# Kernel tuning notes

Measured on AMD Instinct MI355X. Metric: run time of the kernel, lower is better.

The kernel has to match this reference:

```python
import jax, jax.numpy as jnp
import numpy as np
from jax.ops import segment_sum, segment_max

N_NODES, N_EDGES, D_IN, D_H, D_E, HEADS, LAYERS, D_OUT, N_GRAPHS = 50000, 150000, 48, 64, 16, 10, 3, 128, 4096


def setup_inputs() -> dict:
    key = jax.random.key(0)
    ks = jax.random.split(key, 24)
    x = jax.random.normal(ks[0], (N_NODES, D_IN), jnp.float32)
    edge_attr = jax.random.uniform(ks[1], (N_EDGES, D_E), jnp.float32)
    edge_index = jax.random.randint(ks[2], (2, N_EDGES), 0, N_NODES, dtype=jnp.int32)
    batch_ids = jnp.sort(jax.random.randint(ks[3], (N_NODES,), 0, N_GRAPHS, dtype=jnp.int32))
    s = 0.05
    W_emb = jax.random.normal(ks[4], (D_IN, D_H), jnp.float32) * s
    b_emb = jnp.zeros((D_H,), jnp.float32)
    Ws = jax.random.normal(ks[5], (LAYERS, D_H, HEADS * D_H), jnp.float32) * s
    att_src = jax.random.normal(ks[6], (LAYERS, HEADS, D_H), jnp.float32) * s
    att_dst = jax.random.normal(ks[7], (LAYERS, HEADS, D_H), jnp.float32) * s
    att_edge = jax.random.normal(ks[8], (LAYERS, HEADS, D_H), jnp.float32) * s
    W_edge = jax.random.normal(ks[9], (LAYERS, D_E, HEADS * D_H), jnp.float32) * s
    bias = jnp.zeros((LAYERS, D_H), jnp.float32)
    bn_gamma = jnp.ones((LAYERS, D_H), jnp.float32)
    bn_beta = jnp.zeros((LAYERS, D_H), jnp.float32)
    bn_mean = jax.random.normal(ks[10], (LAYERS, D_H), jnp.float32) * 0.1
    bn_var = jax.random.uniform(ks[11], (LAYERS, D_H), jnp.float32) + 0.5
    W_out = jax.random.normal(ks[12], (D_H, D_OUT), jnp.float32) * s
    b_out = jnp.zeros((D_OUT,), jnp.float32)
    return dict(x=x, edge_attr=edge_attr, W_emb=W_emb, b_emb=b_emb, Ws=Ws,
                att_src=att_src, att_dst=att_dst, att_edge=att_edge, W_edge=W_edge,
                bias=bias, bn_gamma=bn_gamma, bn_beta=bn_beta, bn_mean=bn_mean,
                bn_var=bn_var, W_out=W_out, b_out=b_out,
                edge_index=edge_index, batch_ids=batch_ids)


def reference(x, edge_attr, W_emb, b_emb, Ws, att_src, att_dst, att_edge, W_edge,
              bias, bn_gamma, bn_beta, bn_mean, bn_var, W_out, b_out,
              edge_index, batch_ids):
    N = x.shape[0]
    H, F = att_src.shape[1], att_src.shape[2]
    src, dst = edge_index[0], edge_index[1]
    # PyG add_self_loops(fill_value='mean'): self-loop edge_attr = scatter-mean of incoming edge_attr
    cnt = segment_sum(jnp.ones(src.shape, jnp.float32), dst, num_segments=N)
    loop_attr = segment_sum(edge_attr, dst, num_segments=N) / jnp.maximum(cnt, 1.0)[:, None]
    ar = jnp.arange(N, dtype=src.dtype)
    src2 = jnp.concatenate([src, ar])
    dst2 = jnp.concatenate([dst, ar])
    ea2 = jnp.concatenate([edge_attr, loop_attr], axis=0)  # [E+N, De]

    h = x @ W_emb + b_emb  # [N, D_H]
    for i in range(Ws.shape[0]):
        xp = (h @ Ws[i]).reshape(N, H, F)                       # [N,H,F]
        a_s = jnp.einsum('nhf,hf->nh', xp, att_src[i])
        a_d = jnp.einsum('nhf,hf->nh', xp, att_dst[i])
        ep = (ea2 @ W_edge[i]).reshape(-1, H, F)                # [E2,H,F]
        a_e = jnp.einsum('ehf,hf->eh', ep, att_edge[i])
        alpha = jax.nn.leaky_relu(a_s[src2] + a_d[dst2] + a_e, 0.2)  # [E2,H]
        m = segment_max(alpha, dst2, num_segments=N)            # segment softmax over dst
        e = jnp.exp(alpha - m[dst2])
        z = segment_sum(e, dst2, num_segments=N)
        att = e / z[dst2]                                       # [E2,H]
        agg = segment_sum(xp[src2] * att[:, :, None], dst2, num_segments=N)  # [N,H,F]
        xc = agg.mean(axis=1) + bias[i]                         # concat=False -> head mean
        xc = (xc - bn_mean[i]) * bn_gamma[i] / jnp.sqrt(bn_var[i] + 1e-5) + bn_beta[i]
        xc = jax.nn.gelu(xc, approximate=False)
        h = h + xc                                              # residual_connection == 'res'
    out = h @ W_out + b_out                                     # [N, D_OUT]
    gsum = segment_sum(out, batch_ids, num_segments=N_GRAPHS)
    gcnt = segment_sum(jnp.ones((N,), jnp.float32), batch_ids, num_segments=N_GRAPHS)
    return gsum / jnp.maximum(gcnt, 1.0)[:, None]               # global_mean_pool [G, D_OUT]
```

## Files before the change

### kernel.cpp

```cpp
#include <hip/hip_runtime.h>
#include <hip/hip_fp16.h>
#include <math.h>

constexpr int NN   = 50000;
constexpr int NE   = 150000;
constexpr int DIN  = 48;
constexpr int DH   = 64;
constexpr int DE   = 16;
constexpr int NHD  = 10;
constexpr int NL   = 3;
constexpr int DOUTC= 128;
constexpr int NG   = 4096;
constexpr int E2   = NE + NN;
constexpr int SCAN_B  = 256;
constexpr int SCAN_NB = (NN + SCAN_B - 1) / SCAN_B;

typedef __bf16 v8bf __attribute__((ext_vector_type(8)));
typedef short  v8s  __attribute__((ext_vector_type(8)));
typedef float  v4f  __attribute__((ext_vector_type(4)));

__device__ inline unsigned short f2bf(float f) {
    unsigned u = __builtin_bit_cast(unsigned, f);
    unsigned r = (u + 0x7FFFu + ((u >> 16) & 1u)) >> 16;
    return (unsigned short)r;
}

__device__ inline v4f MF(v8s a, v8s b, v4f c) {
    return __builtin_amdgcn_mfma_f32_16x16x32_bf16(
        __builtin_bit_cast(v8bf, a), __builtin_bit_cast(v8bf, b), c, 0, 0, 0);
}
__device__ inline v4f MFB(v8bf a, v8s b, v4f c) {
    return __builtin_amdgcn_mfma_f32_16x16x32_bf16(
        a, __builtin_bit_cast(v8bf, b), c, 0, 0, 0);
}

#define RLI(v, l) __builtin_amdgcn_readlane((v), (l))
#define RLH2(v, l) __builtin_bit_cast(__half2, __builtin_amdgcn_readlane(__builtin_bit_cast(int, (v)), (l)))

__global__ void k_zero(int* __restrict__ cnt) {
    int i = blockIdx.x * blockDim.x + threadIdx.x;
    if (i < NN) cnt[i] = 0;
}

__global__ void k_cnt(const int* __restrict__ dst, int* __restrict__ cnt) {
    int e = blockIdx.x * blockDim.x + threadIdx.x;
    if (e < NE) atomicAdd(&cnt[dst[e]], 1);
}

__global__ void k_scan_a(const int* __restrict__ cnt, int* __restrict__ bsum) {
    __shared__ int s[SCAN_B];
    int i = blockIdx.x * SCAN_B + threadIdx.x;
    s[threadIdx.x] = (i < NN) ? (cnt[i] + 1) : 0;
    __syncthreads();
    for (int off = SCAN_B / 2; off > 0; off >>= 1) {
        if (threadIdx.x < off) s[threadIdx.x] += s[threadIdx.x + off];
        __syncthreads();
    }
    if (threadIdx.x == 0) bsum[blockIdx.x] = s[0];
}

__global__ void k_scan_c(const int* __restrict__ cnt, const int* __restrict__ bsum,
                         int* __restrict__ rp, int* __restrict__ cursor) {
    __shared__ int s[SCAN_B];
    __shared__ int boff_s;
    const int t = threadIdx.x;
    int partial = (t < SCAN_NB && t < blockIdx.x) ? bsum[t] : 0;
    s[t] = partial;
    __syncthreads();
    for (int off = SCAN_B / 2; off > 0; off >>= 1) {
        if (t < off) s[t] += s[t + off];
        __syncthreads();
    }
    if (t == 0) boff_s = s[0];
    __syncthreads();
    const int boff = boff_s;
    __syncthreads();
    int i = blockIdx.x * SCAN_B + t;
    if (i < NN) cursor[i] = 0;
    int v = (i < NN) ? (cnt[i] + 1) : 0;
    s[t] = v;
    __syncthreads();
    for (int off = 1; off < SCAN_B; off <<= 1) {
        int tv = (t >= off) ? s[t - off] : 0;
        __syncthreads();
        s[t] += tv;
        __syncthreads();
    }
    if (i < NN) {
        int excl = boff + s[t] - v;
        rp[i] = excl;
        if (i == NN - 1) rp[NN] = excl + v;
    }
}

__global__ void k_csr_fill(const int* __restrict__ src, const int* __restrict__ dst,
                           const int* __restrict__ rp, int* __restrict__ cursor,
                           int* __restrict__ eidx, int* __restrict__ scsr) {
    int e = blockIdx.x * blockDim.x + threadIdx.x;
    if (e >= E2) return;
    int d  = (e < NE) ? dst[e] : (e - NE);
    int sn = (e < NE) ? src[e] : d;
    int pos = atomicAdd(&cursor[d], 1);
    int s = rp[d] + pos;
    eidx[s] = e; scsr[s] = sn;
}

__global__ void k_misc(const int* __restrict__ rp, const int* __restrict__ scsr,
                       const int* __restrict__ eidx, const int* __restrict__ cnt,
                       const float* __restrict__ ea, const int* __restrict__ batch,
                       int* __restrict__ snl12, int* __restrict__ grp,
                       float* __restrict__ loop) {
    int tid = blockIdx.x * blockDim.x + threadIdx.x;
    if (tid < NN * 16) {
        int n = tid >> 4, j = tid & 15;
        int r0 = rp[n], deg = rp[n + 1] - r0;
        int v;
        if (j < 12)      v = (j < deg) ? scsr[r0 + j] : 0;
        else if (j == 12) v = deg;
        else if (j == 13) v = r0;
        else             v = 0;
        snl12[tid] = v;
    } else if (tid < NN * 17) {
        int n = tid - NN * 16;
        int b = batch[n];
        int pb = (n == 0) ? -1 : batch[n - 1];
        for (int g = pb + 1; g <= b; ++g) grp[g] = n;
        if (n == NN - 1) for (int g = b + 1; g <= NG; ++g) grp[g] = NN;
    } else if (tid < NN * 33) {
        int t = tid - NN * 17;
        int n = t >> 4, d = t & 15;
        int r0 = rp[n], r1 = rp[n + 1];
        float s = 0.f;
        for (int q = r0; q < r1; ++q) {
            int eid = eidx[q];
            if (eid < NE) s += ea[(size_t)eid * DE + d];
        }
        int c = cnt[n];
        loop[t] = s * ((c > 1) ? (1.0f / (float)c) : 1.0f);
    }
}

constexpr int N_BTP = NL * 40960;
constexpr int N_WCB = NL * 2048;
constexpr int N_EMB = DH * 64;
constexpr int N_WET = NL * DE * NHD;
__global__ void k_prep(const float* __restrict__ Ws, const float* __restrict__ asrc,
                       const float* __restrict__ adst, const float* __restrict__ We_in,
                       const float* __restrict__ aedge, const float* __restrict__ Wemb,
                       unsigned short* __restrict__ BtP, unsigned short* __restrict__ WcB,
                       unsigned short* __restrict__ BH, unsigned short* __restrict__ BL,
                       float* __restrict__ WeT) {
    int tid = blockIdx.x * blockDim.x + threadIdx.x;
    if (tid < N_BTP) {
        int e  = tid & 7;
        int ln = (tid >> 3) & 63;
        int t  = (tid >> 9) % 20;
        int ct = (tid / 10240) & 3;
        int l  = tid / 40960;
        int f = ct * 16 + (ln & 15);
        int kidx = t * 32 + (ln >> 4) * 8 + e;
        int k = kidx / 10, q = kidx - 10 * (kidx / 10);
        float v = Ws[((size_t)l * DH + k) * 640 + q * 64 + f] * 0.1f;
        BtP[tid] = f2bf(v);
    } else if (tid < N_BTP + N_WCB) {
        int r0 = tid - N_BTP;
        int l = r0 / 2048, r = r0 % 2048;
        int tile = r / 1024, rr = r % 1024;
        int ln = rr / 16, idx = rr % 16;
        int t2 = idx / 8, e = idx % 8;
        int k = t2 * 32 + (ln >> 4) * 8 + e;
        int jc = ln & 15;
        int j = tile * 16 + jc;
        float v = 0.f;
        if (j < 20) {
            int hh = j % NHD;
            const float* a = ((j < NHD) ? asrc : adst) + (size_t)l * NHD * DH + hh * DH;
            const float* w = Ws + ((size_t)l * DH + k) * 640 + hh * DH;
            float s = 0.f;
#pragma unroll
            for (int f = 0; f < DH; ++f) s += w[f] * a[f];
            v = s;
        }
        WcB[r0] = f2bf(v);
    } else if (tid < N_BTP + N_WCB + N_EMB) {
        int r0 = tid - N_BTP - N_WCB;
        int c = r0 >> 6, k = r0 & 63;
        float v = (k < DIN) ? Wemb[(size_t)k * DH + c] : 0.f;
        __bf16 hi = (__bf16)v;
        BH[r0] = __builtin_bit_cast(unsigned short, hi);
        BL[r0] = __builtin_bit_cast(unsigned short, (__bf16)(v - (float)hi));
    } else if (tid < N_BTP + N_WCB + N_EMB + N_WET) {
        int t3 = tid - N_BTP - N_WCB - N_EMB;
        int l = t3 / 160, rr = t3 % 160;
        int hh = rr / 16, d = rr % 16;
        const float* a = aedge + (size_t)l * NHD * DH + hh * DH;
        const float* w = We_in + ((size_t)l * DE + d) * 640 + hh * DH;
        float s = 0.f;
#pragma unroll
        for (int f = 0; f < DH; ++f) s += w[f] * a[f];
        WeT[l * 160 + hh * 16 + d] = s;
    }
}

__global__ void k_ae3(const float* __restrict__ ea, const float* __restrict__ loop,
                      const float* __restrict__ WeT, const int* __restrict__ eidx,
                      __half* __restrict__ aeAll) {
    int tid = blockIdx.x * blockDim.x + threadIdx.x;
    if (tid >= NL * E2 * NHD) return;
    int l = tid / (E2 * NHD);
    int r = tid - l * (E2 * NHD);
    int s = r / NHD, h = r - (r / NHD) * NHD;
    int eid = eidx[s];
    const float* ar = (eid < NE) ? (ea + (size_t)eid * DE) : (loop + (size_t)(eid - NE) * DE);
    const float* wt = WeT + l * 160 + h * 16;
    float4 a0 = *(const float4*)(ar + 0);
    float4 a1 = *(const float4*)(ar + 4);
    float4 a2 = *(const float4*)(ar + 8);
    float4 a3 = *(const float4*)(ar + 12);
    float4 w0 = *(const float4*)(wt + 0);
    float4 w1 = *(const float4*)(wt + 4);
    float4 w2 = *(const float4*)(wt + 8);
    float4 w3 = *(const float4*)(wt + 12);
    float v = a0.x*w0.x + a0.y*w0.y + a0.z*w0.z + a0.w*w0.w
            + a1.x*w1.x + a1.y*w1.y + a1.z*w1.z + a1.w*w1.w
            + a2.x*w2.x + a2.y*w2.y + a2.z*w2.z + a2.w*w2.w
            + a3.x*w3.x + a3.y*w3.y + a3.z*w3.z + a3.w*w3.w;
    aeAll[tid] = (__half)v;
}

__global__ __launch_bounds__(256) void k_emb(const float* __restrict__ x,
        const unsigned short* __restrict__ BH, const unsigned short* __restrict__ BL,
        const float* __restrict__ bemb, const unsigned short* __restrict__ WcB,
        float* __restrict__ h, __half* __restrict__ hh, float* __restrict__ S) {
    __shared__ __align__(16) unsigned short hlb[4][16 * 72];
    const int tid = threadIdx.x;
    const int w = tid >> 6, lane = tid & 63;
    const int la = lane & 15, lb = lane >> 4;
    const int rowbase = blockIdx.x * 64 + w * 16;
    const int nA = rowbase + la;

    v8bf ah[2], al[2];
#pragma unroll
    for (int ks = 0; ks < 2; ++ks) {
        const int k0 = ks * 32 + lb * 8;
        float xv[8];
        if (nA < NN && k0 < DIN) {
            const float* xp = x + (size_t)nA * DIN + k0;
            float4 v0 = *(const float4*)xp;
            float4 v1 = *(const float4*)(xp + 4);
            xv[0]=v0.x; xv[1]=v0.y; xv[2]=v0.z; xv[3]=v0.w;
            xv[4]=v1.x; xv[5]=v1.y; xv[6]=v1.z; xv[7]=v1.w;
        } else {
#pragma unroll
            for (int e = 0; e < 8; ++e) xv[e] = 0.f;
        }
#pragma unroll
        for (int e = 0; e < 8; ++e) {
            __bf16 hi = (__bf16)xv[e];
            ah[ks][e] = hi;
            al[ks][e] = (__bf16)(xv[e] - (float)hi);
        }
    }
    v4f acc[4];
#pragma unroll
    for (int ct = 0; ct < 4; ++ct) acc[ct] = (v4f){0.f, 0.f, 0.f, 0.f};
#pragma unroll
    for (int ct = 0; ct < 4; ++ct) {
#pragma unroll
        for (int ks = 0; ks < 2; ++ks) {
            const int boff = (ct * 16 + la) * 64 + ks * 32 + lb * 8;
            v8s bh = *(const v8s*)&BH[boff];
            v8s bl = *(const v8s*)&BL[boff];
            acc[ct] = MFB(ah[ks], bh, acc[ct]);
            acc[ct] = MFB(al[ks], bh, acc[ct]);
            acc[ct] = MFB(ah[ks], bl, acc[ct]);
        }
    }
#pragma unroll
    for (int ct = 0; ct < 4; ++ct) {
        const int c = ct * 16 + la;
        const float bi = bemb[c];
#pragma unroll
        for (int r = 0; r < 4; ++r) {
            const int row = lb * 4 + r;
            const int n = rowbase + row;
            float v = acc[ct][r] + bi;
            if (n < NN) {
                h[(size_t)n * DH + c] = v;
                hh[(size_t)n * DH + c] = (__half)v;
            }
            hlb[w][row * 72 + c] = f2bf(v);
        }
    }
    __syncthreads();
    v4f s0 = {0.f,0.f,0.f,0.f}, s1 = {0.f,0.f,0.f,0.f};
#pragma unroll
    for (int t = 0; t < 2; ++t) {
        v8s av = *(const v8s*)&hlb[w][la * 72 + t * 32 + lb * 8];
        v8s b0 = *(const v8s*)&WcB[(size_t)(lane) * 16 + t * 8];
        v8s b1 = *(const v8s*)&WcB[(size_t)(64 + lane) * 16 + t * 8];
        s0 = MF(av, b0, s0);
        s1 = MF(av, b1, s1);
    }
#pragma unroll
    for (int r = 0; r < 4; ++r) {
        const int n = rowbase + lb * 4 + r;
        if (n < NN) {
            S[(size_t)n * 20 + la] = s0[r];
            if (la < 4) S[(size_t)n * 20 + 16 + la] = s1[r];
        }
    }
}

__global__ __launch_bounds__(256) void k_layer(
        const float* __restrict__ Sin, const __half* __restrict__ ae,
        __half* __restrict__ wraw,
        const int* __restrict__ snl12, const int* __restrict__ scsr,
        const float* __restrict__ hin, const __half* __restrict__ hinh,
        const unsigned short* __restrict__ BtP, const unsigned short* __restrict__ WcB,
        int do_s, float* __restrict__ Sout,
        const float* __restrict__ bias, const float* __restrict__ gam,
        const float* __restrict__ bet, const float* __restrict__ mean,
        const float* __restrict__ var, float* __restrict__ hout,
        __half* __restrict__ houth) {
    __shared__ __align__(16) unsigned short Gl[16 * 648];
    __shared__ __align__(8)  __half wL[16 * 120];

    const int tid = threadIdx.x;
    const int w = tid >> 6, lane = tid & 63;
    const int blk = blockIdx.x;
    const int nb4 = blk * 16 + w * 4;
    const unsigned* wrawu = (const unsigned*)wraw;

    const int meta = snl12[nb4 * 16 + lane];

    __half hv[4][6];
#pragma unroll
    for (int i = 0; i < 4; ++i) {
#pragma unroll
        for (int j = 0; j < 6; ++j) {
            int sv = RLI(meta, i * 16 + j);
            hv[i][j] = hinh[(size_t)sv * DH + lane];
        }
    }

    if (tid < 160) {
        const int li = tid / 10, h = tid - (tid / 10) * 10;
        const int n = blk * 16 + li;
        const int* mrow = &snl12[n * 16];
        const int deg = mrow[12];
        const int r0  = mrow[13];
        const float sd = Sin[(size_t)n * 20 + 10 + h];
        float aL[12];
        float m = -1e30f;
#pragma unroll
        for (int s = 0; s < 12; ++s) {
            float a = -1e30f;
            if (s < deg) {
                int sn = mrow[s];
                a = Sin[(size_t)sn * 20 + h] + sd + (float)ae[(size_t)(r0 + s) * NHD + h];
                a = (a > 0.f) ? a : 0.2f * a;
                m = fmaxf(m, a);
            }
            aL[s] = a;
        }
        for (int s = 12; s < deg; ++s) {
            int sn = scsr[r0 + s];
            float a = Sin[(size_t)sn * 20 + h] + sd + (float)ae[(size_t)(r0 + s) * NHD + h];
            a = (a > 0.f) ? a : 0.2f * a;
            wraw[(size_t)(r0 + s) * NHD + h] = (__half)a;
            m = fmaxf(m, a);
        }
        float z = 0.f;
#pragma unroll
        for (int s = 0; s < 12; ++s) {
            float e = (s < deg) ? __expf(aL[s] - m) : 0.f;
            aL[s] = e;
            z += e;
        }
        for (int s = 12; s < deg; ++s) {
            float e = __expf((float)wraw[(size_t)(r0 + s) * NHD + h] - m);
            wraw[(size_t)(r0 + s) * NHD + h] = (__half)e;
            z += e;
        }
        float zi = 1.f / z;
#pragma unroll
        for (int s = 0; s < 12; ++s)
            wL[li * 120 + s * 10 + h] = (__half)(aL[s] * zi);
        for (int s = 12; s < deg; ++s)
            wraw[(size_t)(r0 + s) * NHD + h] =
                (__half)((float)wraw[(size_t)(r0 + s) * NHD + h] * zi);
    }
    __syncthreads();

    const unsigned* wLu = (const unsigned*)wL;
    int wfu[4];
#pragma unroll
    for (int i = 0; i < 4; ++i)
        wfu[i] = (int)wLu[(w * 4 + i) * 60 + (lane & 31)];
#pragma unroll
    for (int i = 0; i < 4; ++i) {
        const int li = w * 4 + i;
        const int deg = RLI(meta, i * 16 + 12);
        const int r0  = RLI(meta, i * 16 + 13);
        __half2 g[5];
#pragma unroll
        for (int p = 0; p < 5; ++p) g[p] = __half2{(__half)0.f, (__half)0.f};
#pragma unroll
        for (int j = 0; j < 6; ++j) {
            __half2 hvd = __half2half2(hv[i][j]);
#pragma unroll
            for (int p = 0; p < 5; ++p)
                g[p] = __hfma2(RLH2(wfu[i], j * 5 + p), hvd, g[p]);
        }
        if (deg > 6) {
            {
                int w2 = (lane < 30) ? (int)wLu[li * 60 + 30 + lane] : 0;
                __half hv2[6];
#pragma unroll
                for (int j = 0; j < 6; ++j) {
                    int sv = RLI(meta, i * 16 + 6 + j);
                    hv2[j] = hinh[(size_t)sv * DH + lane];
                }
#pragma unroll
                for (int j = 0; j < 6; ++j) {
                    __half2 hvd = __half2half2(hv2[j]);
#pragma unroll
                    for (int p = 0; p < 5; ++p)
                        g[p] = __hfma2(RLH2(w2, j * 5 + p), hvd, g[p]);
                }
            }
            for (int c0 = 12; c0 < deg; c0 += 6) {
                const int rem = deg - c0;
                int w2 = (lane < 30 && (lane / 5) < rem)
                         ? (int)wrawu[(size_t)(r0 + c0) * 5 + lane] : 0;
                int s2 = (lane < 6 && c0 + lane < deg) ? scsr[r0 + c0 + lane] : 0;
                __half hv2[6];
#pragma unroll
                for (int j = 0; j < 6; ++j) {
                    int sv = RLI(s2, j);
                    hv2[j] = hinh[(size_t)sv * DH + lane];
                }
#pragma unroll
                for (int j = 0; j < 6; ++j) {
                    __half2 hvd = __half2half2(hv2[j]);
#pragma unroll
                    for (int p = 0; p < 5; ++p)
                        g[p] = __hfma2(RLH2(w2, j * 5 + p), hvd, g[p]);
                }
            }
        }
        const int base = li * 648 + lane * 10;
#pragma unroll
        for (int p = 0; p < 5; ++p) {
            float f0 = __low2float(g[p]), f1 = __high2float(g[p]);
            unsigned u = (unsigned)f2bf(f0) | ((unsigned)f2bf(f1) << 16);
            *(unsigned*)&Gl[base + 2 * p] = u;
        }
    }
    __syncthreads();

    const int la = lane & 15, lb = lane >> 4;
    v4f acc = {0.f, 0.f, 0.f, 0.f};
    const unsigned short* bp = BtP + (size_t)w * 20 * 512;
#pragma unroll 5
    for (int t = 0; t < 20; ++t) {
        v8s av = *(const v8s*)&Gl[la * 648 + t * 32 + lb * 8];
        v8s bv = *(const v8s*)&bp[t * 512 + lane * 8];
        acc = MF(av, bv, acc);
    }
    __syncthreads();

    unsigned short* hlb = Gl;
    const int f = w * 16 + la;
    const float bi = bias[f], gm = gam[f], bt_ = bet[f], mu = mean[f];
    const float iv = rsqrtf(var[f] + 1e-5f);
#pragma unroll
    for (int r = 0; r < 4; ++r) {
        const int local = lb * 4 + r;
        const int n = blk * 16 + local;
        float hvold = hin[(size_t)n * DH + f];
        float v = acc[r] + bi;
        v = (v - mu) * gm * iv + bt_;
        v = 0.5f * v * (1.0f + erff(v * 0.70710678118654752f));
        float hnew = hvold + v;
        hout[(size_t)n * DH + f] = hnew;
        houth[(size_t)n * DH + f] = (__half)hnew;
        hlb[local * 72 + f] = f2bf(hnew);
    }

    if (do_s) {
        __syncthreads();
        if (w < 2) {
            v4f sa = {0.f, 0.f, 0.f, 0.f};
#pragma unroll
            for (int t = 0; t < 2; ++t) {
                v8s av = *(const v8s*)&hlb[la * 72 + t * 32 + lb * 8];
                v8s bv = *(const v8s*)&WcB[(size_t)(w * 64 + lane) * 16 + t * 8];
                sa = MF(av, bv, sa);
            }
#pragma unroll
            for (int r = 0; r < 4; ++r) {
                const int n = blk * 16 + lb * 4 + r;
                if (w == 0) Sout[(size_t)n * 20 + la] = sa[r];
                else if (la < 4) Sout[(size_t)n * 20 + 16 + la] = sa[r];
            }
        }
    }
}

__global__ __launch_bounds__(256) void k_gout(const float* __restrict__ h,
        const float* __restrict__ W, const float* __restrict__ b,
        const int* __restrict__ grp, float* __restrict__ out) {
    __shared__ float Wl[DH * DOUTC];
    __shared__ float hl[4][DH];
    __shared__ float cl[4];
    for (int i = threadIdx.x; i < DH * DOUTC; i += 256) Wl[i] = W[i];
    int w = threadIdx.x >> 6, lane = threadIdx.x & 63;
    int g = blockIdx.x * 4 + w;
    int r0 = grp[g], r1 = grp[g + 1];
    float s = 0.f;
    for (int n = r0; n < r1; ++n) s += h[(size_t)n * DH + lane];
    hl[w][lane] = s;
    if (lane == 0) cl[w] = (float)(r1 - r0);
    __syncthreads();
    for (int idx = threadIdx.x; idx < 4 * DOUTC; idx += 256) {
        int gi = idx >> 7, c = idx & 127;
        float cnt = cl[gi];
        float inv = 1.f / fmaxf(cnt, 1.f);
        float acc = cnt * b[c];
        const float* hr = hl[gi];
#pragma unroll 16
        for (int k = 0; k < DH; ++k) acc += hr[k] * Wl[k * DOUTC + c];
        out[(size_t)(blockIdx.x * 4 + gi) * DOUTC + c] = acc * inv;
    }
}

extern "C" void kernel_launch(void* const* d_in, const int* in_sizes, int n_in,
                              void* d_out, int out_size, void* d_ws, size_t ws_size,
                              hipStream_t stream) {
    const float* x        = (const float*)d_in[0];
    const float* edge_attr= (const float*)d_in[1];
    const float* W_emb    = (const float*)d_in[2];
    const float* b_emb    = (const float*)d_in[3];
    const float* Ws       = (const float*)d_in[4];
    const float* att_src  = (const float*)d_in[5];
    const float* att_dst  = (const float*)d_in[6];
    const float* att_edge = (const float*)d_in[7];
    const float* W_edge   = (const float*)d_in[8];
    const float* bias     = (const float*)d_in[9];
    const float* bn_gamma = (const float*)d_in[10];
    const float* bn_beta  = (const float*)d_in[11];
    const float* bn_mean  = (const float*)d_in[12];
    const float* bn_var   = (const float*)d_in[13];
    const float* W_out    = (const float*)d_in[14];
    const float* b_out    = (const float*)d_in[15];
    const int*   srcp     = (const int*)d_in[16];
    const int*   dstp     = srcp + NE;
    const int*   batch    = (const int*)d_in[17];
    float* out = (float*)d_out;

    char* wsb = (char*)d_ws;
    size_t off = 0;
    auto alloc = [&](size_t bytes) -> void* {
        void* p = (void*)(wsb + off);
        off += (bytes + 255) & ~(size_t)255;
        return p;
    };
    float*  h0    = (float*)alloc((size_t)NN * DH * 4);
    float*  h1    = (float*)alloc((size_t)NN * DH * 4);
    __half* hh0   = (__half*)alloc((size_t)NN * DH * 2);
    __half* hh1   = (__half*)alloc((size_t)NN * DH * 2);
    float*  S0    = (float*)alloc((size_t)NN * 20 * 4);
    float*  S1    = (float*)alloc((size_t)NN * 20 * 4);
    __half* wraw  = (__half*)alloc((size_t)E2 * NHD * 2);
    __half* aeAll = (__half*)alloc((size_t)NL * E2 * NHD * 2);
    float*  loop  = (float*)alloc((size_t)NN * DE * 4);
    int*    cnt   = (int*)alloc((size_t)NN * 4);
    int*    rp    = (int*)alloc((size_t)(NN + 1) * 4);
    int*    cursor= (int*)alloc((size_t)NN * 4);
    int*    eidx  = (int*)alloc((size_t)E2 * 4);
    int*    scsr  = (int*)alloc((size_t)E2 * 4);
    int*    snl12 = (int*)alloc((size_t)NN * 16 * 4);
    int*    bsum  = (int*)alloc((size_t)SCAN_NB * 4);
    int*    grp   = (int*)alloc((size_t)(NG + 1) * 4);
    float*  WeT   = (float*)alloc((size_t)NL * 160 * 4);
    unsigned short* BtP = (unsigned short*)alloc((size_t)NL * 40960 * 2);
    unsigned short* WcB = (unsigned short*)alloc((size_t)NL * 2048 * 2);
    unsigned short* BH  = (unsigned short*)alloc((size_t)DH * 64 * 2);
    unsigned short* BL  = (unsigned short*)alloc((size_t)DH * 64 * 2);

    k_zero<<<(NN + 255) / 256, 256, 0, stream>>>(cnt);
    k_cnt<<<(NE + 255) / 256, 256, 0, stream>>>(dstp, cnt);
    k_scan_a<<<SCAN_NB, SCAN_B, 0, stream>>>(cnt, bsum);
    k_scan_c<<<SCAN_NB, SCAN_B, 0, stream>>>(cnt, bsum, rp, cursor);
    k_csr_fill<<<(E2 + 255) / 256, 256, 0, stream>>>(srcp, dstp, rp, cursor, eidx, scsr);
    k_misc<<<(NN * 33 + 255) / 256, 256, 0, stream>>>(rp, scsr, eidx, cnt, edge_attr,
                                                      batch, snl12, grp, loop);

    k_prep<<<(N_BTP + N_WCB + N_EMB + N_WET + 255) / 256, 256, 0, stream>>>(
        Ws, att_src, att_dst, W_edge, att_edge, W_emb, BtP, WcB, BH, BL, WeT);
    k_ae3<<<(NL * E2 * NHD + 255) / 256, 256, 0, stream>>>(edge_attr, loop, WeT, eidx, aeAll);

    k_emb<<<(NN + 63) / 64, 256, 0, stream>>>(x, BH, BL, b_emb, WcB, h0, hh0, S0);

    float*  hb[2]  = {h0, h1};
    __half* hhb[2] = {hh0, hh1};
    float*  Sb[2]  = {S0, S1};
    for (int l = 0; l < NL; ++l) {
        float*  hin   = hb[l & 1];
        float*  hout  = hb[(l + 1) & 1];
        __half* hinh  = hhb[l & 1];
        __half* houth = hhb[(l + 1) & 1];
        float*  Sin   = Sb[l & 1];
        float*  Sout  = Sb[(l + 1) & 1];
        k_layer<<<NN / 16, 256, 0, stream>>>(
            Sin, aeAll + (size_t)l * E2 * NHD, wraw, snl12, scsr, hin, hinh,
            BtP + (size_t)l * 40960,
            WcB + (size_t)(l + 1 < NL ? l + 1 : 0) * 2048,
            (l + 1 < NL) ? 1 : 0, Sout,
            bias + l * DH, bn_gamma + l * DH, bn_beta + l * DH,
            bn_mean + l * DH, bn_var + l * DH, hout, houth);
    }
    float* hfin = hb[NL & 1];

    k_gout<<<NG / 4, 256, 0, stream>>>(hfin, W_out, b_out, grp, out);
}
```

Before: 223.4 us.

## Compute attention logits per edge with vector loads and make softmax wave-local

The first phase now assigns one lane per (node, edge-slot) pair within each wave. Each lane loads the ten source and destination head scores and the edge logits as vectors, applies leaky ReLU, and stages the results in shared memory. A second phase lets each wave do the per-head softmax for its own four nodes, so the block-wide __syncthreads becomes a wave barrier. The intent is to replace strided scalar gathers done by 160 threads with coalesced vector loads and to remove block-level synchronisation. The cost is extra shared-memory traffic in the Gl buffer, and correctness relies on each wave touching only its own rows of wL and Gl.

```diff
diff --git a/kernel.cpp b/kernel.cpp
--- a/kernel.cpp
+++ b/kernel.cpp
@@ -344,32 +344,73 @@
         }
     }
 
-    if (tid < 160) {
-        const int li = tid / 10, h = tid - (tid / 10) * 10;
-        const int n = blk * 16 + li;
-        const int* mrow = &snl12[n * 16];
-        const int deg = mrow[12];
-        const int r0  = mrow[13];
-        const float sd = Sin[(size_t)n * 20 + 10 + h];
+    const int i0a = (lane < 48) ? (lane / 12) : 0;
+    const int s0a = (lane < 48) ? (lane - i0a * 12) : 0;
+    const int sn_a  = __shfl(meta, i0a * 16 + s0a);
+    const int deg_a = __shfl(meta, i0a * 16 + 12);
+    const int r0_a  = __shfl(meta, i0a * 16 + 13);
+
+    if (lane < 48 && s0a < deg_a) {
+        const int li = w * 4 + i0a;
+        const int n  = nb4 + i0a;
+        const float* sr = Sin + (size_t)sn_a * 20;
+        const float* dr = Sin + (size_t)n * 20 + 10;
+        const unsigned* aer = (const unsigned*)ae + (size_t)(r0_a + s0a) * 5;
+        float4 t0 = *(const float4*)sr;
+        float4 t1 = *(const float4*)(sr + 4);
+        float2 t2 = *(const float2*)(sr + 8);
+        float2 d0 = *(const float2*)(dr + 0);
+        float2 d1 = *(const float2*)(dr + 2);
+        float2 d2 = *(const float2*)(dr + 4);
+        float2 d3 = *(const float2*)(dr + 6);
+        float2 d4 = *(const float2*)(dr + 8);
+        unsigned ew[5];
+#pragma unroll
+        for (int p = 0; p < 5; ++p) ew[p] = aer[p];
+        float as_[10] = {t0.x,t0.y,t0.z,t0.w,t1.x,t1.y,t1.z,t1.w,t2.x,t2.y};
+        float sd_[10] = {d0.x,d0.y,d1.x,d1.y,d2.x,d2.y,d3.x,d3.y,d4.x,d4.y};
+        float* aSrow = (float*)&Gl[li * 648];
+#pragma unroll
+        for (int p = 0; p < 5; ++p) {
+            __half2 eh = __builtin_bit_cast(__half2, ew[p]);
+            float a0 = as_[2*p]   + sd_[2*p]   + __low2float(eh);
+            float a1 = as_[2*p+1] + sd_[2*p+1] + __high2float(eh);
+            a0 = (a0 > 0.f) ? a0 : 0.2f * a0;
+            a1 = (a1 > 0.f) ? a1 : 0.2f * a1;
+            float2 fp = {a0, a1};
+            *(float2*)&aSrow[s0a * 10 + 2 * p] = fp;
+        }
+    }
+    __builtin_amdgcn_wave_barrier();
+
+    const int i0b = (lane < 40) ? (lane / 10) : 0;
+    const int h_b = (lane < 40) ? (lane - i0b * 10) : 0;
+    const int deg_b = __shfl(meta, i0b * 16 + 12);
+    const int r0_b  = __shfl(meta, i0b * 16 + 13);
+
+    if (lane < 40) {
+        const int i0 = i0b, h = h_b;
+        const int li = w * 4 + i0;
+        const int n = nb4 + i0;
+        const int deg = deg_b, r0 = r0_b;
+        const float* aSrow = (const float*)&Gl[li * 648];
         float aL[12];
         float m = -1e30f;
 #pragma unroll
         for (int s = 0; s < 12; ++s) {
             float a = -1e30f;
-            if (s < deg) {
-                int sn = mrow[s];
-                a = Sin[(size_t)sn * 20 + h] + sd + (float)ae[(size_t)(r0 + s) * NHD + h];
+            if (s < deg) { a = aSrow[s * 10 + h]; m = fmaxf(m, a); }
+            aL[s] = a;
+        }
+        if (deg > 12) {
+            const float sd = Sin[(size_t)n * 20 + 10 + h];
+            for (int s = 12; s < deg; ++s) {
+                int sn = scsr[r0 + s];
+                float a = Sin[(size_t)sn * 20 + h] + sd + (float)ae[(size_t)(r0 + s) * NHD + h];
                 a = (a > 0.f) ? a : 0.2f * a;
+                wraw[(size_t)(r0 + s) * NHD + h] = (__half)a;
                 m = fmaxf(m, a);
             }
-            aL[s] = a;
-        }
-        for (int s = 12; s < deg; ++s) {
-            int sn = scsr[r0 + s];
-            float a = Sin[(size_t)sn * 20 + h] + sd + (float)ae[(size_t)(r0 + s) * NHD + h];
-            a = (a > 0.f) ? a : 0.2f * a;
-            wraw[(size_t)(r0 + s) * NHD + h] = (__half)a;
-            m = fmaxf(m, a);
         }
         float z = 0.f;
 #pragma unroll
@@ -391,7 +432,7 @@
             wraw[(size_t)(r0 + s) * NHD + h] =
                 (__half)((float)wraw[(size_t)(r0 + s) * NHD + h] * zi);
     }
-    __syncthreads();
+    __builtin_amdgcn_wave_barrier();
 
     const unsigned* wLu = (const unsigned*)wL;
     int wfu[4];
```

New measurement: 199.2 us. 1.12x faster.
